# Optimization experiments

Hardware: AMD Instinct MI355X
Metric: run time of the kernel (lower is better)

Reference implementation:

```python
import jax, jax.numpy as jnp
import numpy as np

H, D, E, S_E, P_E, N, B = 16, 48, 768, 384, 128, 768, 1

def _ln(x, g=None, b=None, eps=1e-5):
    mu = jnp.mean(x, axis=-1, keepdims=True)
    var = jnp.var(x, axis=-1, keepdims=True)
    y = (x - mu) * jax.lax.rsqrt(var + eps)
    if g is not None:
        y = y * g
    if b is not None:
        y = y + b
    return y

def setup_inputs() -> dict:
    key = jax.random.key(0)
    ks = jax.random.split(key, 16)
    sc_e = 1.0 / np.sqrt(E)
    sc_s = 1.0 / np.sqrt(S_E)
    sc_p = 1.0 / np.sqrt(P_E)
    return {
        "a": jax.random.normal(ks[0], (B, N, E), jnp.float32),
        "s": jax.random.normal(ks[1], (B, N, S_E), jnp.float32),
        "pair_rep": jax.random.normal(ks[2], (B, N, N, P_E), jnp.float32),
        "beta": jax.random.normal(ks[3], (B, N, N), jnp.float32),
        # AdaLN: sigmoid-gated scale and shift from s
        "w_ada_gamma": jax.random.normal(ks[4], (S_E, E), jnp.float32) * sc_s,
        "w_ada_beta": jax.random.normal(ks[5], (S_E, E), jnp.float32) * sc_s,
        # q/k/v projections, stored as [E, H, D]
        "wq": jax.random.normal(ks[6], (E, H, D), jnp.float32) * sc_e,
        "bq": jnp.zeros((H, D), jnp.float32),
        "wk": jax.random.normal(ks[7], (E, H, D), jnp.float32) * sc_e,
        "wv": jax.random.normal(ks[8], (E, H, D), jnp.float32) * sc_e,
        # pair bias: LayerNorm(P_E) + Linear(P_E -> H, no bias)
        "ln_pair_g": jnp.ones((P_E,), jnp.float32),
        "ln_pair_b": jnp.zeros((P_E,), jnp.float32),
        "w_pair": jax.random.normal(ks[9], (P_E, H), jnp.float32) * sc_p,
        # gate projection [E, H, D], no bias, sigmoid
        "w_gate": jax.random.normal(ks[10], (E, H, D), jnp.float32) * sc_e,
        # output projections
        "w_proj_a": jax.random.normal(ks[11], (E, E), jnp.float32) * sc_e,
        "w_out": jax.random.normal(ks[12], (S_E, E), jnp.float32) * sc_s,
        "b_out": jnp.full((E,), -2.0, jnp.float32),
    }

def reference(a, s, pair_rep, beta, w_ada_gamma, w_ada_beta, wq, bq, wk, wv,
              ln_pair_g, ln_pair_b, w_pair, w_gate, w_proj_a, w_out, b_out):
    # AdaLN: normalize a (no affine); gamma/beta conditioned on normalized s
    a_n = _ln(a)
    s_n = _ln(s)
    gamma = jax.nn.sigmoid(s_n @ w_ada_gamma)
    a_mod = gamma * a_n + s_n @ w_ada_beta            # [B,N,E]

    q = jnp.einsum('bne,ehd->bnhd', a_mod, wq) + bq   # [B,N,H,D]
    k = jnp.einsum('bne,ehd->bnhd', a_mod, wk)
    v = jnp.einsum('bne,ehd->bnhd', a_mod, wv)
    g = jax.nn.sigmoid(jnp.einsum('bne,ehd->bnhd', a_mod, w_gate))

    # per-head pair bias: LN(pair) @ w_pair + beta -> [B,H,N,N]
    b = jnp.einsum('bnmp,ph->bhnm', _ln(pair_rep, ln_pair_g, ln_pair_b), w_pair)
    b = b + beta[:, None, :, :]

    scale = 1.0 / np.sqrt(D)
    logits = jnp.einsum('bnhd,bmhd->bhnm', q, k) * scale + b
    weights = jax.nn.softmax(logits, axis=-1)         # [B,H,N,N]

    attn = jnp.einsum('bhnm,bmhd->bhnd', weights, v)
    attn = attn * jnp.moveaxis(g, -2, -3)             # gate per head
    attn = jnp.moveaxis(attn, -3, -2).reshape(a.shape[0], a.shape[1], H * D)
    out = attn @ w_proj_a                             # [B,N,E]
    out = jax.nn.sigmoid(s @ w_out + b_out) * out
    return out
```

## Files before the change

### kernel.cpp

```cpp
#include <hip/hip_runtime.h>
#include <hip/hip_bf16.h>

typedef __attribute__((ext_vector_type(8))) short short8;
typedef __attribute__((ext_vector_type(8))) unsigned short u16x8;
typedef __attribute__((ext_vector_type(4))) unsigned short u16x4;
typedef __attribute__((ext_vector_type(4))) float f32x4;
typedef __attribute__((ext_vector_type(4))) unsigned u32x4;

#define NTOK 768
#define ED   768
#define SD   384
#define PD   128
#define NH   16
#define DH   48
#define LGS  778

__device__ __forceinline__ unsigned short f2bf(float x) {
  unsigned u = __builtin_bit_cast(unsigned, x);
  u += 0x7FFFu + ((u >> 16) & 1u);
  return (unsigned short)(u >> 16);
}
__device__ __forceinline__ float bf2f(unsigned short b) {
  unsigned u = ((unsigned)b) << 16;
  return __builtin_bit_cast(float, u);
}
__device__ __forceinline__ float sigm(float x) { return 1.0f / (1.0f + __expf(-x)); }

__device__ __forceinline__ unsigned cvtpk(float a, float b) {
  unsigned r;
  asm("v_cvt_pk_bf16_f32 %0, %1, %2" : "=v"(r) : "v"(a), "v"(b));
  return r;
}
__device__ __forceinline__ float lo2f(unsigned p) {
  return __builtin_bit_cast(float, p << 16);
}
__device__ __forceinline__ float hi2f(unsigned p) {
  return __builtin_bit_cast(float, p & 0xFFFF0000u);
}

__device__ __forceinline__ void gl2lds(const unsigned short* g, unsigned short* l) {
  __builtin_amdgcn_global_load_lds(
      (const __attribute__((address_space(1))) unsigned int*)g,
      (__attribute__((address_space(3))) unsigned int*)l, 16, 0, 0);
}

constexpr size_t SZ_SN   = (size_t)NTOK * SD * 2;
constexpr size_t OFF_SNH = 0;
constexpr size_t OFF_SNL = OFF_SNH + SZ_SN;
constexpr size_t OFF_SRH = OFF_SNL + SZ_SN;
constexpr size_t OFF_SRL = OFF_SRH + SZ_SN;
constexpr size_t OFF_GAM = OFF_SRL + SZ_SN;
constexpr size_t OFF_BET = OFF_GAM + 2359296;
constexpr size_t OFF_OG  = OFF_BET + 2359296;
constexpr size_t OFF_AMH = OFF_OG  + 2359296;
constexpr size_t OFF_AML = OFF_AMH + 1179648;
constexpr size_t OFF_QB  = OFF_AML + 1179648;
constexpr size_t OFF_KB  = OFF_QB  + 1179648;
constexpr size_t OFF_VT  = OFF_KB  + 1179648;
constexpr size_t OFF_GBUF= OFF_VT  + 1179648;
constexpr size_t OFF_AGH = OFF_GBUF+ 2359296;
constexpr size_t OFF_AGL = OFF_AGH + 1179648;
constexpr size_t OFF_WSMH= OFF_AGL + 1179648;
constexpr size_t OFF_WSML= OFF_WSMH+ 1769472;
constexpr size_t OFF_WQH = OFF_WSML+ 1769472;
constexpr size_t OFF_WQL = OFF_WQH + 4718592;
constexpr size_t OFF_WPH = OFF_WQL + 4718592;
constexpr size_t OFF_WPL = OFF_WPH + 1179648;
constexpr size_t OFF_GWH = OFF_WPL + 1179648;
constexpr size_t OFF_GWL = OFF_GWH + 4096;
constexpr size_t OFF_SGW = OFF_GWL + 4096;
constexpr size_t OFF_QKL = OFF_SGW + 4096;
constexpr size_t OFF_PB  = OFF_QKL + 37748736;
constexpr size_t WS_NEED = OFF_PB  + 18874368;

__global__ __launch_bounds__(256) void k_wcvt(
    const float* __restrict__ wag, const float* __restrict__ wab, const float* __restrict__ wo,
    const float* __restrict__ wq, const float* __restrict__ wk, const float* __restrict__ wv,
    const float* __restrict__ wg, const float* __restrict__ wp,
    const float* __restrict__ lng, const float* __restrict__ lnb,
    const float* __restrict__ wpair, const float* __restrict__ s,
    unsigned short* __restrict__ wsmh, unsigned short* __restrict__ wsml,
    unsigned short* __restrict__ wqh, unsigned short* __restrict__ wql,
    unsigned short* __restrict__ wph, unsigned short* __restrict__ wpl,
    unsigned short* __restrict__ gwh, unsigned short* __restrict__ gwl,
    float* __restrict__ sgw, float* __restrict__ bw,
    unsigned short* __restrict__ snh, unsigned short* __restrict__ snl,
    unsigned short* __restrict__ srh, unsigned short* __restrict__ srl) {
  const int tid = threadIdx.x;
  if (blockIdx.z == 8) {
    const int gid = blockIdx.y * 24 + blockIdx.x;
    if (gid == 192) {
      if (tid < 128) {
        float g = lng[tid];
        for (int hh = 0; hh < 16; ++hh) {
          float gwv = g * wpair[tid * 16 + hh];
          unsigned short hb = f2bf(gwv);
          gwh[tid * 16 + hh] = hb;
          gwl[tid * 16 + hh] = f2bf(gwv - bf2f(hb));
        }
      }
      if (tid < 16) {
        float sv = 0.f, bb = 0.f;
        for (int p = 0; p < 128; ++p) {
          float w = wpair[p * 16 + tid];
          sv += lng[p] * w;
          bb += lnb[p] * w;
        }
        sgw[tid] = sv;
        bw[tid]  = bb;
      }
      return;
    }
    if (gid > 192) return;
    const int n = gid * 4 + (tid >> 6);
    const int lane = tid & 63;
    const float* row = s + (size_t)n * SD;
    float v[6], sum = 0.f, sq = 0.f;
#pragma unroll
    for (int i = 0; i < 6; ++i) { v[i] = row[lane + 64 * i]; sum += v[i]; sq += v[i] * v[i]; }
#pragma unroll
    for (int off = 1; off < 64; off <<= 1) { sum += __shfl_xor(sum, off); sq += __shfl_xor(sq, off); }
    float mu = sum * (1.f / SD);
    float var = sq * (1.f / SD) - mu * mu;
    float rs = rsqrtf(var + 1e-5f);
#pragma unroll
    for (int i = 0; i < 6; ++i) {
      size_t idx = (size_t)n * SD + lane + 64 * i;
      float x = v[i];
      unsigned short xh = f2bf(x);
      srh[idx] = xh; srl[idx] = f2bf(x - bf2f(xh));
      float y = (x - mu) * rs;
      unsigned short yh = f2bf(y);
      snh[idx] = yh; snl[idx] = f2bf(y - bf2f(yh));
    }
    return;
  }
  const int id = blockIdx.z;
  const float* src; int Ksrc; unsigned short *dh, *dl; int n0; int Kd;
  switch (id) {
    case 0: src = wag; Ksrc = 384; dh = wsmh; dl = wsml; n0 = 0;    Kd = 384; break;
    case 1: src = wab; Ksrc = 384; dh = wsmh; dl = wsml; n0 = 768;  Kd = 384; break;
    case 2: src = wo;  Ksrc = 384; dh = wsmh; dl = wsml; n0 = 1536; Kd = 384; break;
    case 3: src = wq;  Ksrc = 768; dh = wqh;  dl = wql;  n0 = 0;    Kd = 768; break;
    case 4: src = wk;  Ksrc = 768; dh = wqh;  dl = wql;  n0 = 768;  Kd = 768; break;
    case 5: src = wv;  Ksrc = 768; dh = wqh;  dl = wql;  n0 = 1536; Kd = 768; break;
    case 6: src = wg;  Ksrc = 768; dh = wqh;  dl = wql;  n0 = 2304; Kd = 768; break;
    default: src = wp; Ksrc = 768; dh = wph;  dl = wpl;  n0 = 0;    Kd = 768; break;
  }
  const int kt = blockIdx.x, ntile = blockIdx.y;
  if (kt * 32 >= Ksrc) return;
  __shared__ float t[32][33];
  const int r = tid >> 3, c4 = (tid & 7) * 4;
  float4 v = *(const float4*)(src + (size_t)(kt * 32 + r) * 768 + ntile * 32 + c4);
  t[r][c4 + 0] = v.x; t[r][c4 + 1] = v.y; t[r][c4 + 2] = v.z; t[r][c4 + 3] = v.w;
  __syncthreads();
  u16x4 hv, lv;
#pragma unroll
  for (int j = 0; j < 4; ++j) {
    float x = t[c4 + j][r];
    unsigned short hb = f2bf(x);
    hv[j] = hb;
    lv[j] = f2bf(x - bf2f(hb));
  }
  size_t drow = (size_t)(n0 + ntile * 32 + r) * Kd + kt * 32 + c4;
  *(u16x4*)(dh + drow) = hv;
  *(u16x4*)(dl + drow) = lv;
}

__device__ __forceinline__ void mfma_core(
    const unsigned short* __restrict__ Ah, const unsigned short* __restrict__ Al,
    const unsigned short* __restrict__ Bh, const unsigned short* __restrict__ Bl,
    int K, int mBase, int nBase, f32x4 acc[2][2]) {
  __shared__ unsigned short lds[2][4][4096];
  const int tid = threadIdx.x;
  const int w = tid >> 6, lane = tid & 63;
  const int l15 = lane & 15, kg = lane >> 4;
  const int wr = w >> 1, wc = w & 1;

  size_t offA[2], offB[2];
  int ldsw[2];
#pragma unroll
  for (int i = 0; i < 2; ++i) {
    int chunk = w * 128 + i * 64 + lane;
    int row = chunk >> 3;
    int slot = (chunk & 7) ^ (row & 7);
    offA[i] = (size_t)(mBase + row) * K + slot * 8;
    offB[i] = (size_t)(nBase + row) * K + slot * 8;
    ldsw[i] = w * 1024 + i * 512;
  }
  auto stage = [&](int b, int k0) {
#pragma unroll
    for (int i = 0; i < 2; ++i) {
      gl2lds(Ah + offA[i] + k0, &lds[b][0][ldsw[i]]);
      gl2lds(Al + offA[i] + k0, &lds[b][1][ldsw[i]]);
      gl2lds(Bh + offB[i] + k0, &lds[b][2][ldsw[i]]);
      gl2lds(Bl + offB[i] + k0, &lds[b][3][ldsw[i]]);
    }
  };

  stage(0, 0);
  int buf = 0;
  for (int k0 = 64; k0 <= K; k0 += 64) {
    __syncthreads();
    if (k0 < K) stage(buf ^ 1, k0);
#pragma unroll
    for (int kk = 0; kk < 2; ++kk) {
      short8 ah[2], al[2], bh4[2], bl4[2];
#pragma unroll
      for (int mi = 0; mi < 2; ++mi) {
        int row = wr * 32 + mi * 16 + l15;
        int kb = kk * 64 + kg * 16;
        int idx = row * 64 + ((kb ^ ((row & 7) << 4)) >> 1);
        ah[mi] = *(const short8*)&lds[buf][0][idx];
        al[mi] = *(const short8*)&lds[buf][1][idx];
      }
#pragma unroll
      for (int ni = 0; ni < 2; ++ni) {
        int row = wc * 32 + ni * 16 + l15;
        int kb = kk * 64 + kg * 16;
        int idx = row * 64 + ((kb ^ ((row & 7) << 4)) >> 1);
        bh4[ni] = *(const short8*)&lds[buf][2][idx];
        bl4[ni] = *(const short8*)&lds[buf][3][idx];
      }
#pragma unroll
      for (int mi = 0; mi < 2; ++mi)
#pragma unroll
        for (int ni = 0; ni < 2; ++ni) {
          acc[mi][ni] = __builtin_amdgcn_mfma_f32_16x16x32_bf16(ah[mi], bh4[ni], acc[mi][ni], 0, 0, 0);
          acc[mi][ni] = __builtin_amdgcn_mfma_f32_16x16x32_bf16(al[mi], bh4[ni], acc[mi][ni], 0, 0, 0);
          acc[mi][ni] = __builtin_amdgcn_mfma_f32_16x16x32_bf16(ah[mi], bl4[ni], acc[mi][ni], 0, 0, 0);
        }
    }
    buf ^= 1;
  }
}

__global__ __launch_bounds__(256) void k_gemm_small(
    const unsigned short* __restrict__ snh, const unsigned short* __restrict__ snl,
    const unsigned short* __restrict__ srh, const unsigned short* __restrict__ srl,
    const unsigned short* __restrict__ wsmh, const unsigned short* __restrict__ wsml,
    const float* __restrict__ bo,
    float* __restrict__ gaml, float* __restrict__ betl, float* __restrict__ og) {
  const int nt = blockIdx.x, mt = blockIdx.y;
  const unsigned short* Ah = (nt < 24) ? snh : srh;
  const unsigned short* Al = (nt < 24) ? snl : srl;
  f32x4 acc[2][2];
#pragma unroll
  for (int i = 0; i < 2; ++i)
#pragma unroll
    for (int j = 0; j < 2; ++j) acc[i][j] = (f32x4){0.f, 0.f, 0.f, 0.f};
  mfma_core(Ah, Al, wsmh, wsml, SD, mt * 64, nt * 64, acc);
  const int tid = threadIdx.x;
  const int w = tid >> 6, lane = tid & 63;
  const int l15 = lane & 15, kg = lane >> 4;
  const int wr = w >> 1, wc = w & 1;
#pragma unroll
  for (int mi = 0; mi < 2; ++mi)
#pragma unroll
    for (int ni = 0; ni < 2; ++ni) {
      int col = nt * 64 + wc * 32 + ni * 16 + l15;
#pragma unroll
      for (int r = 0; r < 4; ++r) {
        int row = mt * 64 + wr * 32 + mi * 16 + kg * 4 + r;
        float v = acc[mi][ni][r];
        if (col < 768) gaml[(size_t)row * ED + col] = v;
        else if (col < 1536) betl[(size_t)row * ED + col - 768] = v;
        else og[(size_t)row * ED + col - 1536] = sigm(v + bo[col - 1536]);
      }
    }
}

__global__ __launch_bounds__(256) void k_gemm_qkvg(
    const unsigned short* __restrict__ amh, const unsigned short* __restrict__ aml,
    const unsigned short* __restrict__ wqh, const unsigned short* __restrict__ wql,
    const float* __restrict__ bq,
    unsigned short* __restrict__ qb, unsigned short* __restrict__ kb,
    unsigned short* __restrict__ vT, float* __restrict__ gbuf) {
  const int nt = blockIdx.x, mt = blockIdx.y;
  f32x4 acc[2][2];
#pragma unroll
  for (int i = 0; i < 2; ++i)
#pragma unroll
    for (int j = 0; j < 2; ++j) acc[i][j] = (f32x4){0.f, 0.f, 0.f, 0.f};
  mfma_core(amh, aml, wqh, wql, ED, mt * 64, nt * 64, acc);
  const int tid = threadIdx.x;
  const int w = tid >> 6, lane = tid & 63;
  const int l15 = lane & 15, kg = lane >> 4;
  const int wr = w >> 1, wc = w & 1;
  const int sel = nt / 12;
#pragma unroll
  for (int mi = 0; mi < 2; ++mi)
#pragma unroll
    for (int ni = 0; ni < 2; ++ni) {
      int col = nt * 64 + wc * 32 + ni * 16 + l15;
      int c = col - sel * 768;
#pragma unroll
      for (int r = 0; r < 4; ++r) {
        int row = mt * 64 + wr * 32 + mi * 16 + kg * 4 + r;
        float v = acc[mi][ni][r];
        size_t idx = (size_t)row * ED + c;
        if (sel == 0) qb[idx] = f2bf(v + bq[c]);
        else if (sel == 1) kb[idx] = f2bf(v);
        else if (sel == 2) vT[(size_t)c * NTOK + row] = f2bf(v);
        else gbuf[idx] = sigm(v);
      }
    }
}

__global__ __launch_bounds__(256) void k_gemm_proj(
    const unsigned short* __restrict__ agh, const unsigned short* __restrict__ agl,
    const unsigned short* __restrict__ wph, const unsigned short* __restrict__ wpl,
    const float* __restrict__ og, float* __restrict__ out) {
  const int nt = blockIdx.x, mt = blockIdx.y;
  f32x4 acc[2][2];
#pragma unroll
  for (int i = 0; i < 2; ++i)
#pragma unroll
    for (int j = 0; j < 2; ++j) acc[i][j] = (f32x4){0.f, 0.f, 0.f, 0.f};
  mfma_core(agh, agl, wph, wpl, ED, mt * 64, nt * 64, acc);
  const int tid = threadIdx.x;
  const int w = tid >> 6, lane = tid & 63;
  const int l15 = lane & 15, kg = lane >> 4;
  const int wr = w >> 1, wc = w & 1;
#pragma unroll
  for (int mi = 0; mi < 2; ++mi)
#pragma unroll
    for (int ni = 0; ni < 2; ++ni) {
      int col = nt * 64 + wc * 32 + ni * 16 + l15;
#pragma unroll
      for (int r = 0; r < 4; ++r) {
        int row = mt * 64 + wr * 32 + mi * 16 + kg * 4 + r;
        size_t idx = (size_t)row * ED + col;
        out[idx] = acc[mi][ni][r] * og[idx];
      }
    }
}

__global__ __launch_bounds__(256) void k_amod(const float* __restrict__ a,
                                              const float* __restrict__ gamma_lin,
                                              const float* __restrict__ beta_lin,
                                              unsigned short* __restrict__ amh,
                                              unsigned short* __restrict__ aml) {
  __shared__ float red[8];
  const int n = blockIdx.x, tid = threadIdx.x;
  const int lane = tid & 63, wid = tid >> 6;
  const float* row = a + (size_t)n * ED;
  float v[3], sum = 0.f, sq = 0.f;
#pragma unroll
  for (int i = 0; i < 3; ++i) { v[i] = row[tid + 256 * i]; sum += v[i]; sq += v[i] * v[i]; }
#pragma unroll
  for (int off = 1; off < 64; off <<= 1) { sum += __shfl_xor(sum, off); sq += __shfl_xor(sq, off); }
  if (lane == 0) { red[wid] = sum; red[4 + wid] = sq; }
  __syncthreads();
  float S = red[0] + red[1] + red[2] + red[3];
  float Q = red[4] + red[5] + red[6] + red[7];
  float mu = S * (1.f / ED);
  float var = Q * (1.f / ED) - mu * mu;
  float rs = rsqrtf(var + 1e-5f);
#pragma unroll
  for (int i = 0; i < 3; ++i) {
    int e = tid + 256 * i;
    float an = (v[i] - mu) * rs;
    size_t idx = (size_t)n * ED + e;
    float val = sigm(gamma_lin[idx]) * an + beta_lin[idx];
    unsigned short h = f2bf(val);
    amh[idx] = h;
    aml[idx] = f2bf(val - bf2f(h));
  }
}

__global__ __launch_bounds__(256) void k_qkw(const unsigned short* __restrict__ qb,
                                             const unsigned short* __restrict__ kb,
                                             const float* __restrict__ beta,
                                             float* __restrict__ qkl) {
  const int mt = blockIdx.x, ntile = blockIdx.y, h = blockIdx.z;
  __shared__ unsigned short qs[128 * 72];
  __shared__ unsigned short ksm[128 * 72];
  const int tid = threadIdx.x;
  const int n0 = ntile * 128, m0 = mt * 128;
  const u16x8 z = {0, 0, 0, 0, 0, 0, 0, 0};
#pragma unroll
  for (int it = 0; it < 4; ++it) {
    int idx = tid + it * 256;
    int row = idx >> 3, c = idx & 7;
    u16x8 vq = z, vk = z;
    if (c < 6) {
      vq = *(const u16x8*)(qb + (size_t)(n0 + row) * ED + h * DH + c * 8);
      vk = *(const u16x8*)(kb + (size_t)(m0 + row) * ED + h * DH + c * 8);
    }
    *(u16x8*)(qs + row * 72 + c * 8) = vq;
    *(u16x8*)(ksm + row * 72 + c * 8) = vk;
  }
  __syncthreads();
  const int w = tid >> 6, lane = tid & 63;
  const int l15 = lane & 15, kg = lane >> 4;
  const int wn = w >> 1, wm = w & 1;
  f32x4 acc[4][4];
#pragma unroll
  for (int i = 0; i < 4; ++i)
#pragma unroll
    for (int j = 0; j < 4; ++j) acc[i][j] = (f32x4){0.f, 0.f, 0.f, 0.f};
#pragma unroll
  for (int ks2 = 0; ks2 < 2; ++ks2) {
    short8 av[4];
#pragma unroll
    for (int ni = 0; ni < 4; ++ni)
      av[ni] = *(const short8*)(qs + (wn * 64 + ni * 16 + l15) * 72 + ks2 * 32 + kg * 8);
#pragma unroll
    for (int mj = 0; mj < 4; ++mj) {
      short8 bv = *(const short8*)(ksm + (wm * 64 + mj * 16 + l15) * 72 + ks2 * 32 + kg * 8);
#pragma unroll
      for (int ni = 0; ni < 4; ++ni)
        acc[ni][mj] = __builtin_amdgcn_mfma_f32_16x16x32_bf16(av[ni], bv, acc[ni][mj], 0, 0, 0);
    }
  }
  const float scale = 0.14433756729740643f;
#pragma unroll
  for (int ni = 0; ni < 4; ++ni)
#pragma unroll
    for (int mj = 0; mj < 4; ++mj)
#pragma unroll
      for (int r = 0; r < 4; ++r) {
        int nn = n0 + wn * 64 + ni * 16 + kg * 4 + r;
        int mm = m0 + wm * 64 + mj * 16 + l15;
        qkl[((size_t)nn * NH + h) * NTOK + mm] =
            fmaf(acc[ni][mj][r], scale, beta[(size_t)nn * NTOK + mm]);
      }
}

__global__ __launch_bounds__(256, 3) void k_pairsm(const float* __restrict__ pair_rep,
                                                   const float* __restrict__ qkl,
                                                   const unsigned short* __restrict__ gw_hi,
                                                   const unsigned short* __restrict__ gw_lo,
                                                   const float* __restrict__ sgw, const float* __restrict__ bw,
                                                   unsigned short* __restrict__ pb) {
  __shared__ float lg[16 * LGS];
  const int n = blockIdx.x;
  const int tid = threadIdx.x;
  const int wv = tid >> 6, lane = tid & 63;
  const int l15 = lane & 15, kg = lane >> 4;

#define LOADCH(X, CH) do {                                                        \
    const float* xp_ = pair_rep + ((size_t)n * NTOK + (CH) * 16 + l15) * PD + kg * 8; \
    _Pragma("unroll")                                                             \
    for (int q_ = 0; q_ < 4; ++q_) {                                              \
      X[q_ * 2]     = *(const float4*)(xp_ + q_ * 32);                            \
      X[q_ * 2 + 1] = *(const float4*)(xp_ + q_ * 32 + 4);                        \
    }                                                                             \
  } while (0)

  float4 Xa[8], Xb[8];
  LOADCH(Xa, wv);
  LOADCH(Xb, wv + 4);

  short8 bh[4], bl[4];
#pragma unroll
  for (int ks = 0; ks < 4; ++ks)
#pragma unroll
    for (int j = 0; j < 8; ++j) {
      int p = ks * 32 + kg * 8 + j;
      bh[ks][j] = (short)gw_hi[p * 16 + l15];
      bl[ks][j] = (short)gw_lo[p * 16 + l15];
    }
  float sgv[4], bwv[4];
#pragma unroll
  for (int r = 0; r < 4; ++r) { sgv[r] = sgw[kg * 4 + r]; bwv[r] = bw[kg * 4 + r]; }

#define PROC(X, CH) do {                                                          \
    float sum_ = 0.f, sq_ = 0.f;                                                  \
    _Pragma("unroll")                                                             \
    for (int q_ = 0; q_ < 8; ++q_) {                                              \
      sum_ += X[q_].x + X[q_].y + X[q_].z + X[q_].w;                              \
      sq_ = fmaf(X[q_].x, X[q_].x, sq_); sq_ = fmaf(X[q_].y, X[q_].y, sq_);       \
      sq_ = fmaf(X[q_].z, X[q_].z, sq_); sq_ = fmaf(X[q_].w, X[q_].w, sq_);       \
    }                                                                             \
    sum_ += __shfl_xor(sum_, 16); sum_ += __shfl_xor(sum_, 32);                   \
    sq_  += __shfl_xor(sq_, 16);  sq_  += __shfl_xor(sq_, 32);                    \
    float mu_ = sum_ * (1.f / 128.f);                                             \
    float rstd_ = rsqrtf(sq_ * (1.f / 128.f) - mu_ * mu_ + 1e-5f);                \
    f32x4 acc_ = {0.f, 0.f, 0.f, 0.f};                                            \
    _Pragma("unroll")                                                             \
    for (int ks_ = 0; ks_ < 4; ++ks_) {                                           \
      float4 u0_ = X[ks_ * 2], u1_ = X[ks_ * 2 + 1];                              \
      unsigned p0_ = cvtpk(u0_.x, u0_.y), p1_ = cvtpk(u0_.z, u0_.w);              \
      unsigned p2_ = cvtpk(u1_.x, u1_.y), p3_ = cvtpk(u1_.z, u1_.w);              \
      float l0_ = u0_.x - lo2f(p0_), l1_ = u0_.y - hi2f(p0_);                     \
      float l2_ = u0_.z - lo2f(p1_), l3_ = u0_.w - hi2f(p1_);                     \
      float l4_ = u1_.x - lo2f(p2_), l5_ = u1_.y - hi2f(p2_);                     \
      float l6_ = u1_.z - lo2f(p3_), l7_ = u1_.w - hi2f(p3_);                     \
      unsigned q0_ = cvtpk(l0_, l1_), q1_ = cvtpk(l2_, l3_);                      \
      unsigned q2_ = cvtpk(l4_, l5_), q3_ = cvtpk(l6_, l7_);                      \
      u32x4 hp_ = {p0_, p1_, p2_, p3_}, lp_ = {q0_, q1_, q2_, q3_};               \
      short8 ah_ = __builtin_bit_cast(short8, hp_);                               \
      short8 al_ = __builtin_bit_cast(short8, lp_);                               \
      acc_ = __builtin_amdgcn_mfma_f32_16x16x32_bf16(bh[ks_], ah_, acc_, 0, 0, 0);\
      acc_ = __builtin_amdgcn_mfma_f32_16x16x32_bf16(bh[ks_], al_, acc_, 0, 0, 0);\
      acc_ = __builtin_amdgcn_mfma_f32_16x16x32_bf16(bl[ks_], ah_, acc_, 0, 0, 0);\
    }                                                                             \
    _Pragma("unroll")                                                             \
    for (int r_ = 0; r_ < 4; ++r_) {                                              \
      float val_ = rstd_ * (acc_[r_] - mu_ * sgv[r_]) + bwv[r_];                  \
      lg[(kg * 4 + r_) * LGS + (CH) * 16 + l15] = val_;                           \
    }                                                                             \
  } while (0)

  PROC(Xa, wv +  0); LOADCH(Xa, wv +  8);
  PROC(Xb, wv +  4); LOADCH(Xb, wv + 12);
  PROC(Xa, wv +  8); LOADCH(Xa, wv + 16);
  PROC(Xb, wv + 12); LOADCH(Xb, wv + 20);
  PROC(Xa, wv + 16); LOADCH(Xa, wv + 24);
  PROC(Xb, wv + 20); LOADCH(Xb, wv + 28);
  PROC(Xa, wv + 24); LOADCH(Xa, wv + 32);
  PROC(Xb, wv + 28); LOADCH(Xb, wv + 36);
  PROC(Xa, wv + 32); LOADCH(Xa, wv + 40);
  PROC(Xb, wv + 36); LOADCH(Xb, wv + 44);
  PROC(Xa, wv + 40);
  PROC(Xb, wv + 44);
#undef LOADCH
#undef PROC
  __syncthreads();

#pragma unroll
  for (int hh = 0; hh < 4; ++hh) {
    int h = wv * 4 + hh;
    const float* qrow = qkl + ((size_t)n * NH + h) * NTOK;
    float x[12];
#pragma unroll
    for (int i = 0; i < 12; ++i) x[i] = lg[h * LGS + lane + 64 * i] + qrow[lane + 64 * i];
    float mx = x[0];
#pragma unroll
    for (int t = 1; t < 12; ++t) mx = fmaxf(mx, x[t]);
#pragma unroll
    for (int off = 1; off < 64; off <<= 1) mx = fmaxf(mx, __shfl_xor(mx, off));
    float e[12], sm = 0.f;
#pragma unroll
    for (int t = 0; t < 12; ++t) { e[t] = __expf(x[t] - mx); sm += e[t]; }
#pragma unroll
    for (int off = 1; off < 64; off <<= 1) sm += __shfl_xor(sm, off);
    float inv = 1.0f / sm;
    unsigned short* dst = pb + ((size_t)h * NTOK + n) * NTOK;
#pragma unroll
    for (int i = 0; i < 12; ++i) dst[lane + 64 * i] = f2bf(e[i] * inv);
  }
}

__global__ __launch_bounds__(64) void k_pv(const unsigned short* __restrict__ wb,
                                           const unsigned short* __restrict__ vT,
                                           const float* __restrict__ gbuf,
                                           unsigned short* __restrict__ agh,
                                           unsigned short* __restrict__ agl) {
  const int nt16 = blockIdx.x, h = blockIdx.y;
  const int n0 = nt16 * 16;
  const int lane = threadIdx.x;
  const int l15 = lane & 15, kg = lane >> 4;
  f32x4 acc[3];
#pragma unroll
  for (int dt = 0; dt < 3; ++dt) acc[dt] = (f32x4){0.f, 0.f, 0.f, 0.f};
  const unsigned short* prow = wb + ((size_t)h * NTOK + n0 + l15) * NTOK + kg * 8;
  const unsigned short* vrow0 = vT + (size_t)(h * DH + l15) * NTOK + kg * 8;
  for (int k0 = 0; k0 < NTOK; k0 += 64) {
#pragma unroll
    for (int ks2 = 0; ks2 < 2; ++ks2) {
      int kofs = k0 + ks2 * 32;
      short8 av = *(const short8*)(prow + kofs);
#pragma unroll
      for (int dt = 0; dt < 3; ++dt) {
        short8 bv = *(const short8*)(vrow0 + (size_t)dt * 16 * NTOK + kofs);
        acc[dt] = __builtin_amdgcn_mfma_f32_16x16x32_bf16(av, bv, acc[dt], 0, 0, 0);
      }
    }
  }
#pragma unroll
  for (int dt = 0; dt < 3; ++dt)
#pragma unroll
    for (int r = 0; r < 4; ++r) {
      int nn = n0 + kg * 4 + r;
      int col = h * DH + dt * 16 + l15;
      size_t idx = (size_t)nn * ED + col;
      float val = acc[dt][r] * gbuf[idx];
      unsigned short hb = f2bf(val);
      agh[idx] = hb;
      agl[idx] = f2bf(val - bf2f(hb));
    }
}

extern "C" void kernel_launch(void* const* d_in, const int* in_sizes, int n_in,
                              void* d_out, int out_size, void* d_ws, size_t ws_size,
                              hipStream_t stream) {
  const float* a    = (const float*)d_in[0];
  const float* s    = (const float*)d_in[1];
  const float* pair = (const float*)d_in[2];
  const float* beta = (const float*)d_in[3];
  const float* wag  = (const float*)d_in[4];
  const float* wab  = (const float*)d_in[5];
  const float* wq   = (const float*)d_in[6];
  const float* bq   = (const float*)d_in[7];
  const float* wk   = (const float*)d_in[8];
  const float* wvp  = (const float*)d_in[9];
  const float* lng  = (const float*)d_in[10];
  const float* lnb  = (const float*)d_in[11];
  const float* wpair= (const float*)d_in[12];
  const float* wg   = (const float*)d_in[13];
  const float* wproj= (const float*)d_in[14];
  const float* wo   = (const float*)d_in[15];
  const float* bo   = (const float*)d_in[16];
  float* out = (float*)d_out;

  if (ws_size < WS_NEED) return;

  char* ws = (char*)d_ws;
  unsigned short* snh  = (unsigned short*)(ws + OFF_SNH);
  unsigned short* snl  = (unsigned short*)(ws + OFF_SNL);
  unsigned short* srh  = (unsigned short*)(ws + OFF_SRH);
  unsigned short* srl  = (unsigned short*)(ws + OFF_SRL);
  float*          gaml = (float*)(ws + OFF_GAM);
  float*          betl = (float*)(ws + OFF_BET);
  float*          og   = (float*)(ws + OFF_OG);
  unsigned short* amh  = (unsigned short*)(ws + OFF_AMH);
  unsigned short* aml  = (unsigned short*)(ws + OFF_AML);
  unsigned short* qb   = (unsigned short*)(ws + OFF_QB);
  unsigned short* kb   = (unsigned short*)(ws + OFF_KB);
  unsigned short* vT   = (unsigned short*)(ws + OFF_VT);
  float*          gbuf = (float*)(ws + OFF_GBUF);
  unsigned short* agh  = (unsigned short*)(ws + OFF_AGH);
  unsigned short* agl  = (unsigned short*)(ws + OFF_AGL);
  unsigned short* wsmh = (unsigned short*)(ws + OFF_WSMH);
  unsigned short* wsml = (unsigned short*)(ws + OFF_WSML);
  unsigned short* wqh  = (unsigned short*)(ws + OFF_WQH);
  unsigned short* wql  = (unsigned short*)(ws + OFF_WQL);
  unsigned short* wph  = (unsigned short*)(ws + OFF_WPH);
  unsigned short* wpl  = (unsigned short*)(ws + OFF_WPL);
  unsigned short* gwh  = (unsigned short*)(ws + OFF_GWH);
  unsigned short* gwl  = (unsigned short*)(ws + OFF_GWL);
  float*          sgw  = (float*)(ws + OFF_SGW);
  float*          bw   = sgw + 16;
  float*          qkl  = (float*)(ws + OFF_QKL);
  unsigned short* pb   = (unsigned short*)(ws + OFF_PB);

  hipLaunchKernelGGL(k_wcvt, dim3(24, 24, 9), dim3(256), 0, stream,
                     wag, wab, wo, wq, wk, wvp, wg, wproj, lng, lnb, wpair, s,
                     wsmh, wsml, wqh, wql, wph, wpl, gwh, gwl, sgw, bw,
                     snh, snl, srh, srl);
  hipLaunchKernelGGL(k_gemm_small, dim3(36, 12), dim3(256), 0, stream,
                     snh, snl, srh, srl, wsmh, wsml, bo, gaml, betl, og);
  hipLaunchKernelGGL(k_amod, dim3(768), dim3(256), 0, stream, a, gaml, betl, amh, aml);
  hipLaunchKernelGGL(k_gemm_qkvg, dim3(48, 12), dim3(256), 0, stream,
                     amh, aml, wqh, wql, bq, qb, kb, vT, gbuf);
  hipLaunchKernelGGL(k_qkw, dim3(6, 6, 16), dim3(256), 0, stream, qb, kb, beta, qkl);
  hipLaunchKernelGGL(k_pairsm, dim3(768), dim3(256), 0, stream,
                     pair, qkl, gwh, gwl, sgw, bw, pb);
  hipLaunchKernelGGL(k_pv, dim3(48, 16), dim3(64), 0, stream, pb, vT, gbuf, agh, agl);
  hipLaunchKernelGGL(k_gemm_proj, dim3(12, 12), dim3(256), 0, stream,
                     agh, agl, wph, wpl, og, out);
}
```

Measured before the change: 176.3 us.

## Tile P·V kernel across four waves sharing V tiles through LDS

Restructures the attention-weights-times-V kernel so each 256-thread block covers 64 query rows with four waves. Each k-step stages the weight tile and V tile in LDS, padded to avoid bank conflicts. All waves then reuse the staged V instead of each wave reading V from global memory. The cost is two block barriers per 32-wide k-step, a grid shrunk from 768 to 192 blocks, and no double buffering, so load latency is exposed.

```diff
diff --git a/kernel.cpp b/kernel.cpp
--- a/kernel.cpp
+++ b/kernel.cpp
@@ -544,37 +544,45 @@
   }
 }
 
-__global__ __launch_bounds__(64) void k_pv(const unsigned short* __restrict__ wb,
-                                           const unsigned short* __restrict__ vT,
-                                           const float* __restrict__ gbuf,
-                                           unsigned short* __restrict__ agh,
-                                           unsigned short* __restrict__ agl) {
-  const int nt16 = blockIdx.x, h = blockIdx.y;
-  const int n0 = nt16 * 16;
-  const int lane = threadIdx.x;
-  const int l15 = lane & 15, kg = lane >> 4;
+__global__ __launch_bounds__(256) void k_pv(const unsigned short* __restrict__ wb,
+                                            const unsigned short* __restrict__ vT,
+                                            const float* __restrict__ gbuf,
+                                            unsigned short* __restrict__ agh,
+                                            unsigned short* __restrict__ agl) {
+  const int ntile = blockIdx.x, h = blockIdx.y;
+  const int n0 = ntile * 64;
+  __shared__ unsigned short wsm[64 * 40];
+  __shared__ unsigned short vtm[48 * 40];
+  const int tid = threadIdx.x;
+  const int wv = tid >> 6, lane = tid & 63, l15 = lane & 15, kg = lane >> 4;
   f32x4 acc[3];
 #pragma unroll
   for (int dt = 0; dt < 3; ++dt) acc[dt] = (f32x4){0.f, 0.f, 0.f, 0.f};
-  const unsigned short* prow = wb + ((size_t)h * NTOK + n0 + l15) * NTOK + kg * 8;
-  const unsigned short* vrow0 = vT + (size_t)(h * DH + l15) * NTOK + kg * 8;
-  for (int k0 = 0; k0 < NTOK; k0 += 64) {
-#pragma unroll
-    for (int ks2 = 0; ks2 < 2; ++ks2) {
-      int kofs = k0 + ks2 * 32;
-      short8 av = *(const short8*)(prow + kofs);
-#pragma unroll
-      for (int dt = 0; dt < 3; ++dt) {
-        short8 bv = *(const short8*)(vrow0 + (size_t)dt * 16 * NTOK + kofs);
-        acc[dt] = __builtin_amdgcn_mfma_f32_16x16x32_bf16(av, bv, acc[dt], 0, 0, 0);
-      }
+  for (int k0 = 0; k0 < NTOK; k0 += 32) {
+    __syncthreads();
+    {
+      int row = tid >> 2, c = tid & 3;
+      *(u16x8*)(wsm + row * 40 + c * 8) =
+          *(const u16x8*)(wb + ((size_t)h * NTOK + (n0 + row)) * NTOK + k0 + c * 8);
+    }
+    if (tid < 192) {
+      int d = tid >> 2, c = tid & 3;
+      *(u16x8*)(vtm + d * 40 + c * 8) =
+          *(const u16x8*)(vT + (size_t)(h * DH + d) * NTOK + k0 + c * 8);
+    }
+    __syncthreads();
+    short8 av = *(const short8*)(wsm + (wv * 16 + l15) * 40 + kg * 8);
+#pragma unroll
+    for (int dt = 0; dt < 3; ++dt) {
+      short8 bv = *(const short8*)(vtm + (dt * 16 + l15) * 40 + kg * 8);
+      acc[dt] = __builtin_amdgcn_mfma_f32_16x16x32_bf16(av, bv, acc[dt], 0, 0, 0);
     }
   }
 #pragma unroll
   for (int dt = 0; dt < 3; ++dt)
 #pragma unroll
     for (int r = 0; r < 4; ++r) {
-      int nn = n0 + kg * 4 + r;
+      int nn = n0 + wv * 16 + kg * 4 + r;
       int col = h * DH + dt * 16 + l15;
       size_t idx = (size_t)nn * ED + col;
       float val = acc[dt][r] * gbuf[idx];
@@ -649,7 +657,7 @@
   hipLaunchKernelGGL(k_qkw, dim3(6, 6, 16), dim3(256), 0, stream, qb, kb, beta, qkl);
   hipLaunchKernelGGL(k_pairsm, dim3(768), dim3(256), 0, stream,
                      pair, qkl, gwh, gwl, sgw, bw, pb);
-  hipLaunchKernelGGL(k_pv, dim3(48, 16), dim3(64), 0, stream, pb, vT, gbuf, agh, agl);
+  hipLaunchKernelGGL(k_pv, dim3(12, 16), dim3(256), 0, stream, pb, vT, gbuf, agh, agl);
   hipLaunchKernelGGL(k_gemm_proj, dim3(12, 12), dim3(256), 0, stream,
                      agh, agl, wph, wpl, og, out);
 }
```

After: 182.4 us. 1.03x slower.
